# Optimization experiments

Hardware: AMD Instinct MI355X
Metric: run time of the kernel (lower is better)

Reference implementation:

```python
import jax, jax.numpy as jnp
import numpy as np

B, N, DIM, H, DK, DV = 2, 2048, 1536, 8, 64, 192


def relative_shift(x):
    # x: [b, h, t1, 2*t1-1] -> [b, h, t1, t1] via Transformer-XL pad/reshape trick
    b, h, t1, t2 = x.shape
    x = jnp.pad(x, ((0, 0), (0, 0), (0, 0), (1, 0)))  # prepend zero column
    t2p = t2 + 1
    x = x.reshape(b, h, t2p, t1)
    x = x[:, :, 1:, :].reshape(b, h, t1, t2)
    return x[..., : (t2p + 1) // 2]


def setup_inputs() -> dict:
    key = jax.random.key(0)
    ks = jax.random.split(key, 9)
    s = 0.02
    return {
        "x": jax.random.normal(ks[0], (B, N, DIM), jnp.float32),
        "Wq": jax.random.normal(ks[1], (DIM, H * DK), jnp.float32) * s,
        "Wk": jax.random.normal(ks[2], (DIM, H * DK), jnp.float32) * s,
        "Wv": jax.random.normal(ks[3], (DIM, H * DV), jnp.float32) * s,
        "W_rel": jax.random.normal(ks[4], (1, H * DK), jnp.float32) * s,
        "Wo": jax.random.normal(ks[5], (H * DV, DIM), jnp.float32) * s,
        "bo": jnp.zeros((DIM,), jnp.float32),
        "rel_content_bias": jax.random.normal(ks[6], (1, H, 1, DK), jnp.float32),
        "rel_pos_bias": jax.random.normal(ks[7], (1, H, 1, DK), jnp.float32),
    }


def reference(x, Wq, Wk, Wv, W_rel, Wo, bo, rel_content_bias, rel_pos_bias):
    b, n, _ = x.shape
    scale = DK ** -0.5
    split = lambda t, d: t.reshape(b, n, H, d).transpose(0, 2, 1, 3)  # b h n d
    q = split(x @ Wq, DK) * scale
    k = split(x @ Wk, DK)
    v = split(x @ Wv, DV)

    content_logits = jnp.einsum("bhid,bhjd->bhij", q + rel_content_bias, k)

    distances = jnp.arange(-n + 1, n, dtype=jnp.float32)[:, None]  # [2n-1, 1]
    rel_k = (distances @ W_rel).reshape(2 * n - 1, H, DK).transpose(1, 0, 2)  # h j d
    rel_logits = jnp.einsum("bhid,hjd->bhij", q + rel_pos_bias, rel_k)
    rel_logits = relative_shift(rel_logits)

    attn = jax.nn.softmax(content_logits + rel_logits, axis=-1)
    out = jnp.einsum("bhij,bhjd->bhid", attn, v)
    out = out.transpose(0, 2, 1, 3).reshape(b, n, H * DV)
    return out @ Wo + bo
```

## Files before the change

kernel.cpp:

```cpp
#include <hip/hip_runtime.h>
#include <math.h>

typedef __attribute__((ext_vector_type(8))) short short8;
typedef __attribute__((ext_vector_type(4))) float floatx4;

namespace {
constexpr int kB = 2, kN = 2048, kDIM = 1536, kH = 8, kDK = 64, kDV = 192;
constexpr int kHDV = kH * kDV;
constexpr float kScale = 0.125f;
}

__device__ __forceinline__ unsigned short f2b(float f) {
    union { float f; unsigned u; } v; v.f = f;
    unsigned r = (v.u + 0x7FFFu + ((v.u >> 16) & 1u)) >> 16;
    return (unsigned short)r;
}

__global__ __launch_bounds__(256) void conv_w(
    const float* __restrict__ src, unsigned short* __restrict__ dst, int Ncols)
{
    __shared__ float Ts[32][33];
    const int tx = threadIdx.x & 31, ty = threadIdx.x >> 5;
    const int k0 = blockIdx.x * 32, n0 = blockIdx.y * 32;
#pragma unroll
    for (int p = 0; p < 4; ++p)
        Ts[ty + p * 8][tx] = src[(size_t)(k0 + ty + p * 8) * Ncols + n0 + tx];
    __syncthreads();
#pragma unroll
    for (int p = 0; p < 4; ++p)
        dst[(size_t)(n0 + ty + p * 8) * kDIM + k0 + tx] = f2b(Ts[tx][ty + p * 8]);
}

__global__ __launch_bounds__(256) void conv_x(
    const float* __restrict__ x, unsigned short* __restrict__ xb)
{
    int idx = blockIdx.x * 256 + threadIdx.x;
    float4 v = *(const float4*)&x[(size_t)idx * 4];
    ushort4 o; o.x = f2b(v.x); o.y = f2b(v.y); o.z = f2b(v.z); o.w = f2b(v.w);
    *(ushort4*)&xb[(size_t)idx * 4] = o;
}

__global__ __launch_bounds__(256) void wcm_pre(
    const float* __restrict__ Wq, const float* __restrict__ Wrel,
    const float* __restrict__ rpb, float* __restrict__ wcm)
{
    int gid = blockIdx.x * 256 + threadIdx.x;
    if (gid < 12288) {
        int dim = gid >> 3, h = gid & 7;
        float s = 0.f;
#pragma unroll 8
        for (int d = 0; d < 64; ++d)
            s += Wq[(size_t)dim * 512 + h * 64 + d] * Wrel[h * 64 + d];
        wcm[h * kDIM + dim] = s * kScale;
    } else if (gid < 12296) {
        int h = gid - 12288;
        float s = 0.f;
#pragma unroll 8
        for (int d = 0; d < 64; ++d) s += rpb[h * 64 + d] * Wrel[h * 64 + d];
        wcm[12288 + h] = s;
    }
}

__global__ __launch_bounds__(256) void c_gemm(
    const float* __restrict__ x, const float* __restrict__ wcm,
    float* __restrict__ cw)
{
    const int row  = blockIdx.x * 4 + (threadIdx.x >> 6);
    const int lane = threadIdx.x & 63;
    const float* xr = x + (size_t)row * kDIM;

    float4 xv[6];
#pragma unroll
    for (int c = 0; c < 6; ++c)
        xv[c] = *(const float4*)&xr[c * 256 + lane * 4];

    float acc[8];
#pragma unroll
    for (int h = 0; h < 8; ++h) {
        const float* wr = wcm + h * kDIM;
        float a = 0.f;
#pragma unroll
        for (int c = 0; c < 6; ++c) {
            float4 wv = *(const float4*)&wr[c * 256 + lane * 4];
            a += xv[c].x * wv.x + xv[c].y * wv.y + xv[c].z * wv.z + xv[c].w * wv.w;
        }
        acc[h] = a;
    }
#pragma unroll
    for (int h = 0; h < 8; ++h) {
        float a = acc[h];
        a += __shfl_xor(a, 1, 64);
        a += __shfl_xor(a, 2, 64);
        a += __shfl_xor(a, 4, 64);
        a += __shfl_xor(a, 8, 64);
        a += __shfl_xor(a, 16, 64);
        a += __shfl_xor(a, 32, 64);
        acc[h] = a;
    }
    if (lane == 0) {
        const int b = row >> 11, i = row & 2047;
#pragma unroll
        for (int h = 0; h < 8; ++h)
            cw[(size_t)(b * 8 + h) * kN + i] = acc[h] + wcm[12288 + h];
    }
}

__global__ __launch_bounds__(256) void mm_qkv(
    const unsigned short* __restrict__ xb,
    const unsigned short* __restrict__ wt,
    const float* __restrict__ rcb,
    unsigned short* __restrict__ qo,
    unsigned short* __restrict__ ko,
    unsigned short* __restrict__ vo)
{
    __shared__ unsigned short A_lds[128 * 72];
    __shared__ unsigned short B_lds[128 * 72];
    const int tid = threadIdx.x;
    const int wave = tid >> 6, lane = tid & 63, lm = lane & 15, lg = lane >> 4;
    const int bm = blockIdx.y * 128, bn = blockIdx.x * 128;
    const int mb = (wave >> 1) * 64, nb = (wave & 1) * 64;

    floatx4 acc[4][4];
#pragma unroll
    for (int i = 0; i < 4; ++i)
#pragma unroll
        for (int j = 0; j < 4; ++j)
#pragma unroll
            for (int r = 0; r < 4; ++r) acc[i][j][r] = 0.f;

    const int srow = tid >> 3, scc = (tid & 7) * 8;
    short8 ra[4], rb[4];
#pragma unroll
    for (int p = 0; p < 4; ++p) {
        ra[p] = *(const short8*)&xb[(size_t)(bm + srow + p * 32) * kDIM + scc];
        rb[p] = *(const short8*)&wt[(size_t)(bn + srow + p * 32) * kDIM + scc];
    }

    for (int kt = 0; kt < 24; ++kt) {
        __syncthreads();
#pragma unroll
        for (int p = 0; p < 4; ++p) {
            *(short8*)&A_lds[(srow + p * 32) * 72 + scc] = ra[p];
            *(short8*)&B_lds[(srow + p * 32) * 72 + scc] = rb[p];
        }
        __syncthreads();
        if (kt < 23) {
            int k0 = (kt + 1) * 64;
#pragma unroll
            for (int p = 0; p < 4; ++p) {
                ra[p] = *(const short8*)&xb[(size_t)(bm + srow + p * 32) * kDIM + k0 + scc];
                rb[p] = *(const short8*)&wt[(size_t)(bn + srow + p * 32) * kDIM + k0 + scc];
            }
        }
#pragma unroll
        for (int ks = 0; ks < 2; ++ks) {
            short8 af[4], bf[4];
#pragma unroll
            for (int mi = 0; mi < 4; ++mi)
                af[mi] = *(const short8*)&A_lds[(mb + mi * 16 + lm) * 72 + lg * 8 + 32 * ks];
#pragma unroll
            for (int ni = 0; ni < 4; ++ni)
                bf[ni] = *(const short8*)&B_lds[(nb + ni * 16 + lm) * 72 + lg * 8 + 32 * ks];
#pragma unroll
            for (int mi = 0; mi < 4; ++mi)
#pragma unroll
                for (int ni = 0; ni < 4; ++ni)
                    acc[mi][ni] = __builtin_amdgcn_mfma_f32_16x16x32_bf16(
                        af[mi], bf[ni], acc[mi][ni], 0, 0, 0);
        }
    }

#pragma unroll
    for (int mi = 0; mi < 4; ++mi)
#pragma unroll
        for (int ni = 0; ni < 4; ++ni)
#pragma unroll
            for (int r = 0; r < 4; ++r) {
                int row = bm + mb + mi * 16 + lg * 4 + r;
                int b = row >> 11, i = row & 2047;
                int col = bn + nb + ni * 16 + lm;
                float v = acc[mi][ni][r];
                if (bn < 512) {
                    int h = col >> 6, d = col & 63;
                    qo[((size_t)(b * 8 + h) * kN + i) * kDK + d] =
                        f2b(v * kScale + rcb[h * 64 + d]);
                } else if (bn < 1024) {
                    int c2 = col - 512, h = c2 >> 6, d = c2 & 63;
                    ko[((size_t)(b * 8 + h) * kN + i) * kDK + d] = f2b(v);
                } else {
                    int c2 = col - 1024, h = c2 / 192, d = c2 - h * 192;
                    vo[((size_t)(b * 8 + h) * kN + i) * kDV + d] = f2b(v);
                }
            }
}

__global__ __launch_bounds__(256) void vtrans(
    const unsigned short* __restrict__ vw, unsigned short* __restrict__ vt)
{
    __shared__ unsigned short Ts[32][33];
    const int tx = threadIdx.x & 31, ty = threadIdx.x >> 5;
    const int i0 = blockIdx.x * 32, d0 = blockIdx.y * 32, bh = blockIdx.z;
#pragma unroll
    for (int p = 0; p < 4; ++p)
        Ts[ty + p * 8][tx] = vw[((size_t)bh * kN + i0 + ty + p * 8) * kDV + d0 + tx];
    __syncthreads();
#pragma unroll
    for (int p = 0; p < 4; ++p)
        vt[((size_t)bh * kDV + d0 + ty + p * 8) * kN + i0 + tx] = Ts[tx][ty + p * 8];
}

__global__ __launch_bounds__(256) void flash_attn(
    const unsigned short* __restrict__ q,
    const unsigned short* __restrict__ k,
    const unsigned short* __restrict__ vt,
    const float* __restrict__ crel,
    unsigned short* __restrict__ ao)
{
    __shared__ unsigned short K_lds[64 * 72];
    __shared__ unsigned short V_lds[192 * 72];
    __shared__ unsigned short P_lds[4 * 16 * 72];
    __shared__ float cs[64];

    const int tid = threadIdx.x;
    const int wave = tid >> 6, lane = tid & 63, lm = lane & 15, lg = lane >> 4;
    const int bh = blockIdx.y;
    const int i0 = blockIdx.x * 64;

    short8 qA[2];
    {
        const size_t qb = ((size_t)bh * kN + i0 + wave * 16 + lm) * kDK + lg * 8;
        qA[0] = *(const short8*)&q[qb];
        qA[1] = *(const short8*)&q[qb + 32];
    }
    if (tid < 64) cs[tid] = crel[(size_t)bh * kN + i0 + tid];

    floatx4 o4[12];
#pragma unroll
    for (int nd = 0; nd < 12; ++nd)
#pragma unroll
        for (int r = 0; r < 4; ++r) o4[nd][r] = 0.f;
    float m_[4] = {-INFINITY, -INFINITY, -INFINITY, -INFINITY};
    float l_[4] = {0.f, 0.f, 0.f, 0.f};

    const unsigned short* kb = k + (size_t)bh * kN * kDK;
    const unsigned short* vb = vt + (size_t)bh * kDV * kN;
    const int pbase = wave * 16 * 72;

    for (int t = 0; t < 32; ++t) {
        const int j0 = t * 64;
        __syncthreads();
#pragma unroll
        for (int p = 0; p < 2; ++p) {
            int c = tid + p * 256;
            int row = c >> 3, cc = (c & 7) * 8;
            *(short8*)&K_lds[row * 72 + cc] =
                *(const short8*)&kb[(size_t)(j0 + row) * kDK + cc];
        }
#pragma unroll
        for (int p = 0; p < 6; ++p) {
            int c = tid + p * 256;
            int row = c >> 3, cc = (c & 7) * 8;
            *(short8*)&V_lds[row * 72 + cc] =
                *(const short8*)&vb[(size_t)row * kN + j0 + cc];
        }
        __syncthreads();

        floatx4 s4[4];
#pragma unroll
        for (int st = 0; st < 4; ++st) {
#pragma unroll
            for (int r = 0; r < 4; ++r) s4[st][r] = 0.f;
#pragma unroll
            for (int ks = 0; ks < 2; ++ks) {
                short8 kf = *(const short8*)&K_lds[(st * 16 + lm) * 72 + lg * 8 + 32 * ks];
                s4[st] = __builtin_amdgcn_mfma_f32_16x16x32_bf16(qA[ks], kf, s4[st], 0, 0, 0);
            }
        }

        float alpha[4];
#pragma unroll
        for (int r = 0; r < 4; ++r) {
            const int lrow = wave * 16 + lg * 4 + r;
            const float ci = cs[lrow];
            const float gi = (float)(i0 + lrow);
            float sv[4];
#pragma unroll
            for (int st = 0; st < 4; ++st)
                sv[st] = s4[st][r] + ((float)(j0 + st * 16 + lm) - gi) * ci;
            float mx = fmaxf(fmaxf(sv[0], sv[1]), fmaxf(sv[2], sv[3]));
            mx = fmaxf(mx, __shfl_xor(mx, 1, 64));
            mx = fmaxf(mx, __shfl_xor(mx, 2, 64));
            mx = fmaxf(mx, __shfl_xor(mx, 4, 64));
            mx = fmaxf(mx, __shfl_xor(mx, 8, 64));
            float mnew = fmaxf(m_[r], mx);
            alpha[r] = __expf(m_[r] - mnew);
            m_[r] = mnew;
            float ts = 0.f;
#pragma unroll
            for (int st = 0; st < 4; ++st) {
                float pv = __expf(sv[st] - mnew);
                ts += pv;
                P_lds[pbase + (lg * 4 + r) * 72 + st * 16 + lm] = f2b(pv);
            }
            ts += __shfl_xor(ts, 1, 64);
            ts += __shfl_xor(ts, 2, 64);
            ts += __shfl_xor(ts, 4, 64);
            ts += __shfl_xor(ts, 8, 64);
            l_[r] = l_[r] * alpha[r] + ts;
        }

#pragma unroll
        for (int nd = 0; nd < 12; ++nd)
#pragma unroll
            for (int r = 0; r < 4; ++r) o4[nd][r] *= alpha[r];

        short8 pa[2];
        pa[0] = *(const short8*)&P_lds[pbase + lm * 72 + lg * 8];
        pa[1] = *(const short8*)&P_lds[pbase + lm * 72 + lg * 8 + 32];
#pragma unroll
        for (int nd = 0; nd < 12; ++nd) {
#pragma unroll
            for (int ks = 0; ks < 2; ++ks) {
                short8 vf = *(const short8*)&V_lds[(nd * 16 + lm) * 72 + lg * 8 + 32 * ks];
                o4[nd] = __builtin_amdgcn_mfma_f32_16x16x32_bf16(pa[ks], vf, o4[nd], 0, 0, 0);
            }
        }
    }

    const int b = bh >> 3, h = bh & 7;
#pragma unroll
    for (int r = 0; r < 4; ++r) {
        float inv = 1.f / l_[r];
        size_t rowbase = ((size_t)b * kN + i0 + wave * 16 + lg * 4 + r) * (size_t)kHDV
                         + h * kDV;
#pragma unroll
        for (int nd = 0; nd < 12; ++nd)
            ao[rowbase + nd * 16 + lm] = f2b(o4[nd][r] * inv);
    }
}

__global__ __launch_bounds__(256) void mm_out(
    const unsigned short* __restrict__ aw,
    const unsigned short* __restrict__ wot,
    const float* __restrict__ bias,
    float* __restrict__ out)
{
    __shared__ unsigned short A_lds[128 * 72];
    __shared__ unsigned short B_lds[128 * 72];
    const int tid = threadIdx.x;
    const int wave = tid >> 6, lane = tid & 63, lm = lane & 15, lg = lane >> 4;
    const int bm = blockIdx.y * 128, bn = blockIdx.x * 128;
    const int mb = (wave >> 1) * 64, nb = (wave & 1) * 64;

    floatx4 acc[4][4];
#pragma unroll
    for (int i = 0; i < 4; ++i)
#pragma unroll
        for (int j = 0; j < 4; ++j)
#pragma unroll
            for (int r = 0; r < 4; ++r) acc[i][j][r] = 0.f;

    const int srow = tid >> 3, scc = (tid & 7) * 8;
    short8 ra[4], rb[4];
#pragma unroll
    for (int p = 0; p < 4; ++p) {
        ra[p] = *(const short8*)&aw[(size_t)(bm + srow + p * 32) * kDIM + scc];
        rb[p] = *(const short8*)&wot[(size_t)(bn + srow + p * 32) * kDIM + scc];
    }

    for (int kt = 0; kt < 24; ++kt) {
        __syncthreads();
#pragma unroll
        for (int p = 0; p < 4; ++p) {
            *(short8*)&A_lds[(srow + p * 32) * 72 + scc] = ra[p];
            *(short8*)&B_lds[(srow + p * 32) * 72 + scc] = rb[p];
        }
        __syncthreads();
        if (kt < 23) {
            int k0 = (kt + 1) * 64;
#pragma unroll
            for (int p = 0; p < 4; ++p) {
                ra[p] = *(const short8*)&aw[(size_t)(bm + srow + p * 32) * kDIM + k0 + scc];
                rb[p] = *(const short8*)&wot[(size_t)(bn + srow + p * 32) * kDIM + k0 + scc];
            }
        }
#pragma unroll
        for (int ks = 0; ks < 2; ++ks) {
            short8 af[4], bf[4];
#pragma unroll
            for (int mi = 0; mi < 4; ++mi)
                af[mi] = *(const short8*)&A_lds[(mb + mi * 16 + lm) * 72 + lg * 8 + 32 * ks];
#pragma unroll
            for (int ni = 0; ni < 4; ++ni)
                bf[ni] = *(const short8*)&B_lds[(nb + ni * 16 + lm) * 72 + lg * 8 + 32 * ks];
#pragma unroll
            for (int mi = 0; mi < 4; ++mi)
#pragma unroll
                for (int ni = 0; ni < 4; ++ni)
                    acc[mi][ni] = __builtin_amdgcn_mfma_f32_16x16x32_bf16(
                        af[mi], bf[ni], acc[mi][ni], 0, 0, 0);
        }
    }

#pragma unroll
    for (int mi = 0; mi < 4; ++mi)
#pragma unroll
        for (int ni = 0; ni < 4; ++ni)
#pragma unroll
            for (int r = 0; r < 4; ++r) {
                int row = bm + mb + mi * 16 + lg * 4 + r;
                int col = bn + nb + ni * 16 + lm;
                out[(size_t)row * kDIM + col] = acc[mi][ni][r] + bias[col];
            }
}

extern "C" void kernel_launch(void* const* d_in, const int* in_sizes, int n_in,
                              void* d_out, int out_size, void* d_ws, size_t ws_size,
                              hipStream_t stream)
{
    const float* x    = (const float*)d_in[0];
    const float* Wq   = (const float*)d_in[1];
    const float* Wk   = (const float*)d_in[2];
    const float* Wv   = (const float*)d_in[3];
    const float* Wrel = (const float*)d_in[4];
    const float* Wo   = (const float*)d_in[5];
    const float* bo   = (const float*)d_in[6];
    const float* rcb  = (const float*)d_in[7];
    const float* rpb  = (const float*)d_in[8];
    float* out = (float*)d_out;

    char* w = (char*)d_ws;
    unsigned short* xb  = (unsigned short*)(w);
    unsigned short* wt  = (unsigned short*)(w + 12582912);
    unsigned short* qw  = (unsigned short*)(w + 20447232);
    unsigned short* kw  = (unsigned short*)(w + 24641536);
    unsigned short* vw  = (unsigned short*)(w + 28835840);
    float*          cw  = (float*)(w + 41418752);
    float*          wcm = (float*)(w + 41549824);
    unsigned short* vtp = xb;
    unsigned short* awp = vw;
    unsigned short* wot = wt;

    { dim3 g(48, 16);  conv_w<<<g, 256, 0, stream>>>(Wq, wt,               512); }
    { dim3 g(48, 16);  conv_w<<<g, 256, 0, stream>>>(Wk, wt + 512  * 1536, 512); }
    { dim3 g(48, 48);  conv_w<<<g, 256, 0, stream>>>(Wv, wt + 1024 * 1536, 1536); }
    conv_x<<<6144, 256, 0, stream>>>(x, xb);
    wcm_pre<<<49, 256, 0, stream>>>(Wq, Wrel, rpb, wcm);
    c_gemm<<<1024, 256, 0, stream>>>(x, wcm, cw);

    { dim3 g(20, 32); mm_qkv<<<g, 256, 0, stream>>>(xb, wt, rcb, qw, kw, vw); }

    { dim3 g(48, 48); conv_w<<<g, 256, 0, stream>>>(Wo, wot, 1536); }
    { dim3 g(64, 6, 16); vtrans<<<g, 256, 0, stream>>>(vw, vtp); }

    { dim3 g(32, 16); flash_attn<<<g, 256, 0, stream>>>(qw, kw, vtp, cw, awp); }

    { dim3 g(12, 32); mm_out<<<g, 256, 0, stream>>>(awp, wot, bo, out); }
}
```

Measured before the change: 335.3 us.

## Split PV output columns across waves, use exp2 with log2e folded in, remap blocks

```diff
diff --git a/kernel.cpp b/kernel.cpp
--- a/kernel.cpp
+++ b/kernel.cpp
@@ -8,6 +8,7 @@
 constexpr int kB = 2, kN = 2048, kDIM = 1536, kH = 8, kDK = 64, kDV = 192;
 constexpr int kHDV = kH * kDV;
 constexpr float kScale = 0.125f;
+constexpr float kLog2e = 1.44269504088896340736f;
 }
 
 __device__ __forceinline__ unsigned short f2b(float f) {
@@ -51,13 +52,13 @@
 #pragma unroll 8
         for (int d = 0; d < 64; ++d)
             s += Wq[(size_t)dim * 512 + h * 64 + d] * Wrel[h * 64 + d];
-        wcm[h * kDIM + dim] = s * kScale;
+        wcm[h * kDIM + dim] = s * kScale * kLog2e;
     } else if (gid < 12296) {
         int h = gid - 12288;
         float s = 0.f;
 #pragma unroll 8
         for (int d = 0; d < 64; ++d) s += rpb[h * 64 + d] * Wrel[h * 64 + d];
-        wcm[12288 + h] = s;
+        wcm[12288 + h] = s * kLog2e;
     }
 }
 
@@ -183,7 +184,7 @@
                 if (bn < 512) {
                     int h = col >> 6, d = col & 63;
                     qo[((size_t)(b * 8 + h) * kN + i) * kDK + d] =
-                        f2b(v * kScale + rcb[h * 64 + d]);
+                        f2b((v * kScale + rcb[h * 64 + d]) * kLog2e);
                 } else if (bn < 1024) {
                     int c2 = col - 512, h = c2 >> 6, d = c2 & 63;
                     ko[((size_t)(b * 8 + h) * kN + i) * kDK + d] = f2b(v);
@@ -218,13 +219,17 @@
 {
     __shared__ unsigned short K_lds[64 * 72];
     __shared__ unsigned short V_lds[192 * 72];
-    __shared__ unsigned short P_lds[4 * 16 * 72];
+    __shared__ unsigned short P_lds[64 * 68];
     __shared__ float cs[64];
+    __shared__ float alpha_s[64];
+    __shared__ float l_s[64];
 
     const int tid = threadIdx.x;
     const int wave = tid >> 6, lane = tid & 63, lm = lane & 15, lg = lane >> 4;
-    const int bh = blockIdx.y;
-    const int i0 = blockIdx.x * 64;
+    const int id = blockIdx.x;
+    const int rem = id >> 3;
+    const int bh = (id & 7) * 2 + (rem >> 5);
+    const int i0 = (rem & 31) * 64;
 
     short8 qA[2];
     {
@@ -234,17 +239,18 @@
     }
     if (tid < 64) cs[tid] = crel[(size_t)bh * kN + i0 + tid];
 
-    floatx4 o4[12];
-#pragma unroll
-    for (int nd = 0; nd < 12; ++nd)
-#pragma unroll
-        for (int r = 0; r < 4; ++r) o4[nd][r] = 0.f;
+    floatx4 o4[3][4];
+#pragma unroll
+    for (int nd = 0; nd < 3; ++nd)
+#pragma unroll
+        for (int g = 0; g < 4; ++g)
+#pragma unroll
+            for (int r = 0; r < 4; ++r) o4[nd][g][r] = 0.f;
     float m_[4] = {-INFINITY, -INFINITY, -INFINITY, -INFINITY};
     float l_[4] = {0.f, 0.f, 0.f, 0.f};
 
     const unsigned short* kb = k + (size_t)bh * kN * kDK;
     const unsigned short* vb = vt + (size_t)bh * kDV * kN;
-    const int pbase = wave * 16 * 72;
 
     for (int t = 0; t < 32; ++t) {
         const int j0 = t * 64;
@@ -277,12 +283,11 @@
             }
         }
 
-        float alpha[4];
 #pragma unroll
         for (int r = 0; r < 4; ++r) {
-            const int lrow = wave * 16 + lg * 4 + r;
-            const float ci = cs[lrow];
-            const float gi = (float)(i0 + lrow);
+            const int row = wave * 16 + lg * 4 + r;
+            const float ci = cs[row];
+            const float gi = (float)(i0 + row);
             float sv[4];
 #pragma unroll
             for (int st = 0; st < 4; ++st)
@@ -293,50 +298,71 @@
             mx = fmaxf(mx, __shfl_xor(mx, 4, 64));
             mx = fmaxf(mx, __shfl_xor(mx, 8, 64));
             float mnew = fmaxf(m_[r], mx);
-            alpha[r] = __expf(m_[r] - mnew);
+            float alpha = exp2f(m_[r] - mnew);
             m_[r] = mnew;
             float ts = 0.f;
 #pragma unroll
             for (int st = 0; st < 4; ++st) {
-                float pv = __expf(sv[st] - mnew);
+                float pv = exp2f(sv[st] - mnew);
                 ts += pv;
-                P_lds[pbase + (lg * 4 + r) * 72 + st * 16 + lm] = f2b(pv);
+                P_lds[row * 68 + st * 16 + lm] = f2b(pv);
             }
             ts += __shfl_xor(ts, 1, 64);
             ts += __shfl_xor(ts, 2, 64);
             ts += __shfl_xor(ts, 4, 64);
             ts += __shfl_xor(ts, 8, 64);
-            l_[r] = l_[r] * alpha[r] + ts;
-        }
-
-#pragma unroll
-        for (int nd = 0; nd < 12; ++nd)
-#pragma unroll
-            for (int r = 0; r < 4; ++r) o4[nd][r] *= alpha[r];
-
-        short8 pa[2];
-        pa[0] = *(const short8*)&P_lds[pbase + lm * 72 + lg * 8];
-        pa[1] = *(const short8*)&P_lds[pbase + lm * 72 + lg * 8 + 32];
-#pragma unroll
-        for (int nd = 0; nd < 12; ++nd) {
-#pragma unroll
-            for (int ks = 0; ks < 2; ++ks) {
-                short8 vf = *(const short8*)&V_lds[(nd * 16 + lm) * 72 + lg * 8 + 32 * ks];
-                o4[nd] = __builtin_amdgcn_mfma_f32_16x16x32_bf16(pa[ks], vf, o4[nd], 0, 0, 0);
-            }
-        }
-    }
+            l_[r] = l_[r] * alpha + ts;
+            if (lm == 0) alpha_s[row] = alpha;
+        }
+        __syncthreads();
+
+        floatx4 al[4];
+#pragma unroll
+        for (int g = 0; g < 4; ++g)
+            al[g] = *(const floatx4*)&alpha_s[g * 16 + lg * 4];
+#pragma unroll
+        for (int nd = 0; nd < 3; ++nd)
+#pragma unroll
+            for (int g = 0; g < 4; ++g) o4[nd][g] *= al[g];
+
+#pragma unroll
+        for (int ks = 0; ks < 2; ++ks) {
+            short8 pa[4];
+#pragma unroll
+            for (int g = 0; g < 4; ++g)
+                pa[g] = *(const short8*)&P_lds[(g * 16 + lm) * 68 + lg * 8 + 32 * ks];
+#pragma unroll
+            for (int nd = 0; nd < 3; ++nd) {
+                short8 vf = *(const short8*)&V_lds[(wave * 48 + nd * 16 + lm) * 72 + lg * 8 + 32 * ks];
+#pragma unroll
+                for (int g = 0; g < 4; ++g)
+                    o4[nd][g] = __builtin_amdgcn_mfma_f32_16x16x32_bf16(pa[g], vf, o4[nd][g], 0, 0, 0);
+            }
+        }
+    }
+
+    if (lm == 0) {
+#pragma unroll
+        for (int r = 0; r < 4; ++r) l_s[wave * 16 + lg * 4 + r] = l_[r];
+    }
+    __syncthreads();
+    floatx4 lv[4];
+#pragma unroll
+    for (int g = 0; g < 4; ++g)
+        lv[g] = *(const floatx4*)&l_s[g * 16 + lg * 4];
 
     const int b = bh >> 3, h = bh & 7;
 #pragma unroll
-    for (int r = 0; r < 4; ++r) {
-        float inv = 1.f / l_[r];
-        size_t rowbase = ((size_t)b * kN + i0 + wave * 16 + lg * 4 + r) * (size_t)kHDV
-                         + h * kDV;
-#pragma unroll
-        for (int nd = 0; nd < 12; ++nd)
-            ao[rowbase + nd * 16 + lm] = f2b(o4[nd][r] * inv);
-    }
+    for (int g = 0; g < 4; ++g)
+#pragma unroll
+        for (int r = 0; r < 4; ++r) {
+            float inv = 1.f / lv[g][r];
+            size_t rowbase = ((size_t)b * kN + i0 + g * 16 + lg * 4 + r) * (size_t)kHDV
+                             + h * kDV + wave * 48;
+#pragma unroll
+            for (int nd = 0; nd < 3; ++nd)
+                ao[rowbase + nd * 16 + lm] = f2b(o4[nd][g][r] * inv);
+        }
 }
 
 __global__ __launch_bounds__(256) void mm_out(
@@ -453,7 +479,7 @@
     { dim3 g(48, 48); conv_w<<<g, 256, 0, stream>>>(Wo, wot, 1536); }
     { dim3 g(64, 6, 16); vtrans<<<g, 256, 0, stream>>>(vw, vtp); }
 
-    { dim3 g(32, 16); flash_attn<<<g, 256, 0, stream>>>(qw, kw, vtp, cw, awp); }
+    flash_attn<<<512, 256, 0, stream>>>(qw, kw, vtp, cw, awp);
 
     { dim3 g(12, 32); mm_out<<<g, 256, 0, stream>>>(awp, wot, bo, out); }
 }
```

Result: slower. 395.9 us (+18.1%).
